# Kernel optimization log

Hardware: AMD Instinct MI355X
Metric: run time of the kernel (lower is better)

## Reference

```python
import jax, jax.numpy as jnp
import numpy as np

N_NODES = 50000
N_EDGES = 800000
D_IN = 128
D_OUT = 128


def setup_inputs() -> dict:
    key = jax.random.key(0)
    k1, k2, k3, k4 = jax.random.split(key, 4)
    feature = jax.random.normal(k1, (N_NODES, D_IN), dtype=jnp.float32)
    edge_src = jax.random.randint(k2, (N_EDGES,), 0, N_NODES, dtype=jnp.int32)
    edge_dst = jax.random.randint(k3, (N_EDGES,), 0, N_NODES, dtype=jnp.int32)
    W = jax.random.normal(k4, (D_IN, D_OUT), dtype=jnp.float32) * (1.0 / np.sqrt(D_IN))
    b = jnp.zeros((D_OUT,), dtype=jnp.float32)
    return {"feature": feature, "edge_src": edge_src, "edge_dst": edge_dst, "W": W, "b": b}


def reference(feature, edge_src, edge_dst, W, b):
    # copy_src + sum reduce: for each edge, copy src node feature, sum into dst node
    msgs = feature[edge_src]  # [E, D_IN] gather
    h = jax.ops.segment_sum(msgs, edge_dst, num_segments=N_NODES)  # [N, D_IN]
    # linear + activation (relu)
    return jax.nn.relu(h @ W + b)
```

## Files before the change

### kernel.cpp

```cpp
#include <hip/hip_runtime.h>
#include <hip/hip_fp16.h>


constexpr int N    = 50000;
constexpr int E    = 800000;
constexpr int D    = 128;
constexpr int CAP  = 64;
constexpr int NT   = 3125;
constexpr int ZSTR = 136;
constexpr int NR   = 782;
constexpr int HB   = 500;
constexpr int EPB  = E / HB;

using f16x8 = __attribute__((ext_vector_type(8))) _Float16;
using f32x4 = __attribute__((ext_vector_type(4))) float;

__global__ void setup(const float* __restrict__ W, _Float16* __restrict__ Wf,
                      _Float16* __restrict__ Z) {
    if (blockIdx.x == 8) {
        if (threadIdx.x < D) Z[(size_t)N * D + threadIdx.x] = (_Float16)0.f;
        return;
    }
    int t = blockIdx.x * 256 + threadIdx.x;
    int ct = t >> 8, ks = (t >> 6) & 3, lane = t & 63;
    int q = lane >> 4, li = lane & 15;
    _Float16 v[8];
    #pragma unroll
    for (int j = 0; j < 8; ++j)
        v[j] = (_Float16)W[(ks * 32 + q * 8 + j) * D + ct * 16 + li];
    *(f16x8*)(Wf + (size_t)t * 8) = *(const f16x8*)v;
}

__global__ __launch_bounds__(256) void midk(
        const float* __restrict__ feature,
        const int*   __restrict__ edst,
        const _Float16* __restrict__ Wf,
        int* __restrict__ hist,
        _Float16* __restrict__ Z) {
    __shared__ int h[NR];
    __shared__ _Float16 zs[4][16 * ZSTR];
    const int tid = threadIdx.x;

    if (blockIdx.x < HB) {
        const int b = blockIdx.x;
        for (int i = tid; i < NR; i += 256) h[i] = 0;
        __syncthreads();
        const int e0 = b * EPB;
        for (int i = tid; i < EPB; i += 256)
            atomicAdd(&h[edst[e0 + i] >> 6], 1);
        __syncthreads();
        for (int i = tid; i < NR; i += 256) hist[b * NR + i] = h[i];
        return;
    }

    const int wave = tid >> 6, lane = tid & 63;
    const int wt = (blockIdx.x - HB) * 4 + wave;
    if (wt >= NT) return;
    const int q = lane >> 4, li = lane & 15;

    const float* fp = feature + (size_t)(wt * 16 + li) * D + q * 8;
    f16x8 afr[4];
    #pragma unroll
    for (int ks = 0; ks < 4; ++ks) {
        const float4 u0 = *(const float4*)(fp + ks * 32);
        const float4 u1 = *(const float4*)(fp + ks * 32 + 4);
        afr[ks][0] = (_Float16)u0.x; afr[ks][1] = (_Float16)u0.y;
        afr[ks][2] = (_Float16)u0.z; afr[ks][3] = (_Float16)u0.w;
        afr[ks][4] = (_Float16)u1.x; afr[ks][5] = (_Float16)u1.y;
        afr[ks][6] = (_Float16)u1.z; afr[ks][7] = (_Float16)u1.w;
    }

    f32x4 acc[8];
    #pragma unroll
    for (int ct = 0; ct < 8; ++ct) acc[ct] = (f32x4){0.f, 0.f, 0.f, 0.f};
    #pragma unroll
    for (int ks = 0; ks < 4; ++ks)
        #pragma unroll
        for (int ct = 0; ct < 8; ++ct) {
            const f16x8 b = *(const f16x8*)(Wf + (size_t)((ct * 4 + ks) * 64 + lane) * 8);
            acc[ct] = __builtin_amdgcn_mfma_f32_16x16x32_f16(afr[ks], b, acc[ct], 0, 0, 0);
        }

    _Float16* zt = zs[wave];
    #pragma unroll
    for (int ct = 0; ct < 8; ++ct)
        #pragma unroll
        for (int r = 0; r < 4; ++r)
            zt[(q * 4 + r) * ZSTR + ct * 16 + li] = (_Float16)acc[ct][r];
    #pragma unroll
    for (int it = 0; it < 4; ++it) {
        const f16x8 v = *(const f16x8*)(zt + (it * 4 + q) * ZSTR + li * 8);
        *(f16x8*)(Z + (size_t)(wt * 16 + it * 4 + q) * D + li * 8) = v;
    }
}

__global__ void scank(int* __restrict__ hist, int* __restrict__ total) {
    const int r    = blockIdx.x;
    const int lane = threadIdx.x;
    int h[8], sum = 0;
    #pragma unroll
    for (int j = 0; j < 8; ++j) {
        const int idx = lane * 8 + j;
        h[j] = (idx < HB) ? hist[idx * NR + r] : 0;
        sum += h[j];
    }
    int incl = sum;
    #pragma unroll
    for (int off = 1; off < 64; off <<= 1) {
        int u = __shfl_up(incl, off);
        if (lane >= off) incl += u;
    }
    int run = incl - sum;
    #pragma unroll
    for (int j = 0; j < 8; ++j) {
        const int idx = lane * 8 + j;
        if (idx < HB) hist[idx * NR + r] = run;
        run += h[j];
    }
    if (lane == 63) total[r] = run;
}

__global__ __launch_bounds__(256) void partk(
        const int* __restrict__ esrc,
        const int* __restrict__ edst,
        const int* __restrict__ blockBase,
        const int* __restrict__ total,
        int* __restrict__ rangeStartG,
        unsigned int* __restrict__ part) {
    __shared__ int rs[NR];
    __shared__ int mb[NR];
    __shared__ int rk[NR];
    const int tid = threadIdx.x;
    const int b   = blockIdx.x;

    if (tid < 64) {
        int carry = 0;
        #pragma unroll
        for (int c = 0; c < 13; ++c) {
            const int idx = c * 64 + tid;
            const int v = (idx < NR) ? total[idx] : 0;
            int incl = v;
            #pragma unroll
            for (int off = 1; off < 64; off <<= 1) {
                int u = __shfl_up(incl, off);
                if (tid >= off) incl += u;
            }
            if (idx < NR) rs[idx] = incl - v + carry;
            carry += __shfl(incl, 63);
        }
    }
    for (int i = tid; i < NR; i += 256) { mb[i] = blockBase[b * NR + i]; rk[i] = 0; }
    __syncthreads();
    if (b == 0)
        for (int i = tid; i < NR; i += 256) rangeStartG[i] = rs[i];

    const int e0 = b * EPB;
    for (int i = tid; i < EPB; i += 256) {
        const int s = esrc[e0 + i];
        const int d = edst[e0 + i];
        const int r = d >> 6;
        const int k = atomicAdd(&rk[r], 1);
        part[rs[r] + mb[r] + k] = ((unsigned)(d & 63) << 16) | (unsigned)s;
    }
}

__global__ __launch_bounds__(256) void csrgather(
        const unsigned int* __restrict__ part,
        const int* __restrict__ rangeStart,
        const int* __restrict__ total,
        const _Float16* __restrict__ Z,
        const float* __restrict__ bias,
        float* __restrict__ out) {
    __shared__ unsigned short bkt[64 * CAP];
    __shared__ int deg[64];
    const int r = blockIdx.x, tid = threadIdx.x;

    if (tid < 64) deg[tid] = 0;
    __syncthreads();
    const int rsv = rangeStart[r], tot = total[r];
    for (int i = tid; i < tot; i += 256) {
        const unsigned p = part[rsv + i];
        const int local = p >> 16;
        const int src   = p & 0xFFFF;
        const int k = atomicAdd(&deg[local], 1);
        if (k < CAP) bkt[local * CAP + k] = (unsigned short)src;
    }
    __syncthreads();

    const int wave = tid >> 6, lane = tid & 63;
    const int g = lane >> 4, li = lane & 15;
    const float4 b0 = *(const float4*)(bias + li * 8);
    const float4 b1 = *(const float4*)(bias + li * 8 + 4);

    for (int pair = 0; pair < 8; ++pair) {
        const int lA = wave * 16 + pair * 2;
        const int lB = lA + 1;
        const int degA = min(deg[lA], CAP);
        const int degB = min(deg[lB], CAP);

        float accA[8] = {0,0,0,0,0,0,0,0};
        float accB[8] = {0,0,0,0,0,0,0,0};

        const int mx = max(degA, degB);
        for (int base = 0; base < mx; base += 16) {
            f16x8 hA[4], hB[4];
            #pragma unroll
            for (int t = 0; t < 4; ++t) {
                const int rr = base + t * 4 + g;
                int sA = bkt[lA * CAP + rr];
                int sB = bkt[lB * CAP + rr];
                sA = (rr < degA) ? sA : N;
                sB = (rr < degB) ? sB : N;
                hA[t] = *(const f16x8*)(Z + (size_t)sA * D + li * 8);
                hB[t] = *(const f16x8*)(Z + (size_t)sB * D + li * 8);
            }
            #pragma unroll
            for (int t = 0; t < 4; ++t)
                #pragma unroll
                for (int j = 0; j < 8; ++j) {
                    accA[j] += (float)hA[t][j];
                    accB[j] += (float)hB[t][j];
                }
        }

        #pragma unroll
        for (int j = 0; j < 8; ++j) {
            accA[j] += __shfl_xor(accA[j], 16);
            accA[j] += __shfl_xor(accA[j], 32);
            accB[j] += __shfl_xor(accB[j], 16);
            accB[j] += __shfl_xor(accB[j], 32);
        }

        const int nodeA = (r << 6) + lA;
        const int nodeB = (r << 6) + lB;
        if (g == 0 && nodeA < N) {
            float4 o0, o1;
            o0.x = fmaxf(accA[0] + b0.x, 0.f); o0.y = fmaxf(accA[1] + b0.y, 0.f);
            o0.z = fmaxf(accA[2] + b0.z, 0.f); o0.w = fmaxf(accA[3] + b0.w, 0.f);
            o1.x = fmaxf(accA[4] + b1.x, 0.f); o1.y = fmaxf(accA[5] + b1.y, 0.f);
            o1.z = fmaxf(accA[6] + b1.z, 0.f); o1.w = fmaxf(accA[7] + b1.w, 0.f);
            float* op = out + (size_t)nodeA * D + li * 8;
            *(float4*)op       = o0;
            *(float4*)(op + 4) = o1;
        } else if (g == 1 && nodeB < N) {
            float4 o0, o1;
            o0.x = fmaxf(accB[0] + b0.x, 0.f); o0.y = fmaxf(accB[1] + b0.y, 0.f);
            o0.z = fmaxf(accB[2] + b0.z, 0.f); o0.w = fmaxf(accB[3] + b0.w, 0.f);
            o1.x = fmaxf(accB[4] + b1.x, 0.f); o1.y = fmaxf(accB[5] + b1.y, 0.f);
            o1.z = fmaxf(accB[6] + b1.z, 0.f); o1.w = fmaxf(accB[7] + b1.w, 0.f);
            float* op = out + (size_t)nodeB * D + li * 8;
            *(float4*)op       = o0;
            *(float4*)(op + 4) = o1;
        }
    }
}

extern "C" void kernel_launch(void* const* d_in, const int* in_sizes, int n_in,
                              void* d_out, int out_size, void* d_ws, size_t ws_size,
                              hipStream_t stream) {
    const float* feature = (const float*)d_in[0];
    const int*   esrc    = (const int*)d_in[1];
    const int*   edst    = (const int*)d_in[2];
    const float* W       = (const float*)d_in[3];
    const float* bias    = (const float*)d_in[4];
    float*       out     = (float*)d_out;

    _Float16*     Z      = (_Float16*)d_ws;
    _Float16*     Wf     = Z + (size_t)(N + 1) * D;
    int*          hist   = (int*)(Wf + 16384);
    int*          total  = hist + HB * NR;
    int*          rangeS = total + NR;
    unsigned int* part   = (unsigned int*)(rangeS + NR);

    setup<<<9, 256, 0, stream>>>(W, Wf, Z);
    midk <<<HB + (NT + 3) / 4, 256, 0, stream>>>(feature, edst, Wf, hist, Z);
    scank<<<NR, 64, 0, stream>>>(hist, total);
    partk<<<HB, 256, 0, stream>>>(esrc, edst, hist, total, rangeS, part);
    csrgather<<<NR, 256, 0, stream>>>(part, rangeS, total, Z, bias, out);
}
```

Baseline: 145.1 us.

## Fuse all stages into one cooperative persistent kernel with grid syncs

Replaces the five separate launches (weight setup, histogram+GEMM, scan, partition, CSR gather) with a single cooperative kernel of 512 blocks that separates the phases with grid-wide syncs. Shared memory is unioned across phases, and the histogram is stored transposed so each block can scan one or two ranges. The aim is to remove the gaps and tail effects between dependent kernel launches. In exchange it adds three grid barriers and a fixed grid that handles 782 gather ranges in two uneven rounds, so load balance and occupancy may suffer.

```diff
diff --git a/kernel.cpp b/kernel.cpp
--- a/kernel.cpp
+++ b/kernel.cpp
@@ -1,256 +1,243 @@
 #include <hip/hip_runtime.h>
 #include <hip/hip_fp16.h>
+#include <hip/hip_cooperative_groups.h>
+
+namespace cg = cooperative_groups;
 
 
 constexpr int N    = 50000;
 constexpr int E    = 800000;
 constexpr int D    = 128;
 constexpr int CAP  = 64;
+constexpr int NBLK = 512;
+constexpr int NR   = 782;
 constexpr int NT   = 3125;
 constexpr int ZSTR = 136;
-constexpr int NR   = 782;
-constexpr int HB   = 500;
-constexpr int EPB  = E / HB;
+constexpr int EPB  = 1563;
+constexpr int NCH  = 13;
 
 using f16x8 = __attribute__((ext_vector_type(8))) _Float16;
 using f32x4 = __attribute__((ext_vector_type(4))) float;
 
-__global__ void setup(const float* __restrict__ W, _Float16* __restrict__ Wf,
-                      _Float16* __restrict__ Z) {
-    if (blockIdx.x == 8) {
-        if (threadIdx.x < D) Z[(size_t)N * D + threadIdx.x] = (_Float16)0.f;
-        return;
-    }
-    int t = blockIdx.x * 256 + threadIdx.x;
-    int ct = t >> 8, ks = (t >> 6) & 3, lane = t & 63;
-    int q = lane >> 4, li = lane & 15;
-    _Float16 v[8];
-    #pragma unroll
-    for (int j = 0; j < 8; ++j)
-        v[j] = (_Float16)W[(ks * 32 + q * 8 + j) * D + ct * 16 + li];
-    *(f16x8*)(Wf + (size_t)t * 8) = *(const f16x8*)v;
-}
-
-__global__ __launch_bounds__(256) void midk(
-        const float* __restrict__ feature,
-        const int*   __restrict__ edst,
-        const _Float16* __restrict__ Wf,
-        int* __restrict__ hist,
-        _Float16* __restrict__ Z) {
-    __shared__ int h[NR];
-    __shared__ _Float16 zs[4][16 * ZSTR];
-    const int tid = threadIdx.x;
-
-    if (blockIdx.x < HB) {
-        const int b = blockIdx.x;
-        for (int i = tid; i < NR; i += 256) h[i] = 0;
-        __syncthreads();
-        const int e0 = b * EPB;
-        for (int i = tid; i < EPB; i += 256)
-            atomicAdd(&h[edst[e0 + i] >> 6], 1);
-        __syncthreads();
-        for (int i = tid; i < NR; i += 256) hist[b * NR + i] = h[i];
-        return;
-    }
-
-    const int wave = tid >> 6, lane = tid & 63;
-    const int wt = (blockIdx.x - HB) * 4 + wave;
-    if (wt >= NT) return;
-    const int q = lane >> 4, li = lane & 15;
-
-    const float* fp = feature + (size_t)(wt * 16 + li) * D + q * 8;
-    f16x8 afr[4];
-    #pragma unroll
-    for (int ks = 0; ks < 4; ++ks) {
-        const float4 u0 = *(const float4*)(fp + ks * 32);
-        const float4 u1 = *(const float4*)(fp + ks * 32 + 4);
-        afr[ks][0] = (_Float16)u0.x; afr[ks][1] = (_Float16)u0.y;
-        afr[ks][2] = (_Float16)u0.z; afr[ks][3] = (_Float16)u0.w;
-        afr[ks][4] = (_Float16)u1.x; afr[ks][5] = (_Float16)u1.y;
-        afr[ks][6] = (_Float16)u1.z; afr[ks][7] = (_Float16)u1.w;
-    }
-
-    f32x4 acc[8];
-    #pragma unroll
-    for (int ct = 0; ct < 8; ++ct) acc[ct] = (f32x4){0.f, 0.f, 0.f, 0.f};
-    #pragma unroll
-    for (int ks = 0; ks < 4; ++ks)
-        #pragma unroll
-        for (int ct = 0; ct < 8; ++ct) {
-            const f16x8 b = *(const f16x8*)(Wf + (size_t)((ct * 4 + ks) * 64 + lane) * 8);
-            acc[ct] = __builtin_amdgcn_mfma_f32_16x16x32_f16(afr[ks], b, acc[ct], 0, 0, 0);
-        }
-
-    _Float16* zt = zs[wave];
-    #pragma unroll
-    for (int ct = 0; ct < 8; ++ct)
-        #pragma unroll
-        for (int r = 0; r < 4; ++r)
-            zt[(q * 4 + r) * ZSTR + ct * 16 + li] = (_Float16)acc[ct][r];
-    #pragma unroll
-    for (int it = 0; it < 4; ++it) {
-        const f16x8 v = *(const f16x8*)(zt + (it * 4 + q) * ZSTR + li * 8);
-        *(f16x8*)(Z + (size_t)(wt * 16 + it * 4 + q) * D + li * 8) = v;
-    }
-}
-
-__global__ void scank(int* __restrict__ hist, int* __restrict__ total) {
-    const int r    = blockIdx.x;
-    const int lane = threadIdx.x;
-    int h[8], sum = 0;
-    #pragma unroll
-    for (int j = 0; j < 8; ++j) {
-        const int idx = lane * 8 + j;
-        h[j] = (idx < HB) ? hist[idx * NR + r] : 0;
-        sum += h[j];
-    }
-    int incl = sum;
+__device__ __forceinline__ int wscan_incl(int v, int lane) {
     #pragma unroll
     for (int off = 1; off < 64; off <<= 1) {
-        int u = __shfl_up(incl, off);
-        if (lane >= off) incl += u;
-    }
-    int run = incl - sum;
-    #pragma unroll
-    for (int j = 0; j < 8; ++j) {
-        const int idx = lane * 8 + j;
-        if (idx < HB) hist[idx * NR + r] = run;
-        run += h[j];
-    }
-    if (lane == 63) total[r] = run;
+        int u = __shfl_up(v, off);
+        if (lane >= off) v += u;
+    }
+    return v;
 }
 
-__global__ __launch_bounds__(256) void partk(
-        const int* __restrict__ esrc,
-        const int* __restrict__ edst,
-        const int* __restrict__ blockBase,
-        const int* __restrict__ total,
-        int* __restrict__ rangeStartG,
+__global__ __launch_bounds__(256, 4) void mega(
+        const float* __restrict__ feature,
+        const int*   __restrict__ esrc,
+        const int*   __restrict__ edst,
+        const float* __restrict__ W,
+        const float* __restrict__ bias,
+        float*       __restrict__ out,
+        _Float16*    __restrict__ Z,
+        _Float16*    __restrict__ Wf,
+        int*         __restrict__ histT,
+        int*         __restrict__ mbT,
+        int*         __restrict__ total,
         unsigned int* __restrict__ part) {
     __shared__ int rs[NR];
-    __shared__ int mb[NR];
-    __shared__ int rk[NR];
-    const int tid = threadIdx.x;
-    const int b   = blockIdx.x;
-
-    if (tid < 64) {
+    __shared__ union {
+        int h[NR];
+        _Float16 zs[4][16 * ZSTR];
+        struct { int mb[NR]; int rk[NR]; } c;
+        struct { unsigned short bkt[64 * CAP]; int deg[64]; } d;
+    } sh;
+
+    cg::grid_group grid = cg::this_grid();
+    const int b    = blockIdx.x;
+    const int tid  = threadIdx.x;
+    const int wave = tid >> 6, lane = tid & 63;
+    const int q    = lane >> 4, li = lane & 15;
+    const int e0   = b * EPB;
+    const int ecnt = min(E - e0, EPB);
+
+    if (b < 8) {
+        int t = b * 256 + tid;
+        int ct = t >> 8, ks = (t >> 6) & 3, ln = t & 63;
+        int qq = ln >> 4, ll = ln & 15;
+        _Float16 v[8];
+        #pragma unroll
+        for (int j = 0; j < 8; ++j)
+            v[j] = (_Float16)W[(ks * 32 + qq * 8 + j) * D + ct * 16 + ll];
+        *(f16x8*)(Wf + (size_t)t * 8) = *(const f16x8*)v;
+    }
+    if (b == 8 && tid < D) Z[(size_t)N * D + tid] = (_Float16)0.f;
+
+    for (int i = tid; i < NR; i += 256) sh.h[i] = 0;
+    __syncthreads();
+    for (int i = tid; i < ecnt; i += 256)
+        atomicAdd(&sh.h[edst[e0 + i] >> 6], 1);
+    __syncthreads();
+    for (int i = tid; i < NR; i += 256) histT[i * NBLK + b] = sh.h[i];
+
+    grid.sync();
+
+    #pragma unroll
+    for (int it = 0; it < 2; ++it) {
+        const int wt = it * (NBLK * 4) + b * 4 + wave;
+        if (wt >= NT) break;
+        const float* fp = feature + (size_t)(wt * 16 + li) * D + q * 8;
+        f16x8 afr[4];
+        #pragma unroll
+        for (int ks = 0; ks < 4; ++ks) {
+            const float4 u0 = *(const float4*)(fp + ks * 32);
+            const float4 u1 = *(const float4*)(fp + ks * 32 + 4);
+            afr[ks][0] = (_Float16)u0.x; afr[ks][1] = (_Float16)u0.y;
+            afr[ks][2] = (_Float16)u0.z; afr[ks][3] = (_Float16)u0.w;
+            afr[ks][4] = (_Float16)u1.x; afr[ks][5] = (_Float16)u1.y;
+            afr[ks][6] = (_Float16)u1.z; afr[ks][7] = (_Float16)u1.w;
+        }
+        f32x4 acc[8];
+        #pragma unroll
+        for (int ct = 0; ct < 8; ++ct) acc[ct] = (f32x4){0.f, 0.f, 0.f, 0.f};
+        #pragma unroll
+        for (int ks = 0; ks < 4; ++ks)
+            #pragma unroll
+            for (int ct = 0; ct < 8; ++ct) {
+                const f16x8 bb = *(const f16x8*)(Wf + (size_t)((ct * 4 + ks) * 64 + lane) * 8);
+                acc[ct] = __builtin_amdgcn_mfma_f32_16x16x32_f16(afr[ks], bb, acc[ct], 0, 0, 0);
+            }
+        _Float16* zt = sh.zs[wave];
+        #pragma unroll
+        for (int ct = 0; ct < 8; ++ct)
+            #pragma unroll
+            for (int r = 0; r < 4; ++r)
+                zt[(q * 4 + r) * ZSTR + ct * 16 + li] = (_Float16)acc[ct][r];
+        #pragma unroll
+        for (int jt = 0; jt < 4; ++jt) {
+            const f16x8 v = *(const f16x8*)(zt + (jt * 4 + q) * ZSTR + li * 8);
+            *(f16x8*)(Z + (size_t)(wt * 16 + jt * 4 + q) * D + li * 8) = v;
+        }
+    }
+    if (wave == 0) {
+        #pragma unroll
+        for (int j = 0; j < 2; ++j) {
+            const int r = b + j * NBLK;
+            if (r >= NR) break;
+            int carry = 0;
+            #pragma unroll
+            for (int c = 0; c < NBLK / 64; ++c) {
+                const int idx = c * 64 + lane;
+                const int v = histT[r * NBLK + idx];
+                const int incl = wscan_incl(v, lane);
+                mbT[idx * NR + r] = incl - v + carry;
+                carry += __shfl(incl, 63);
+            }
+            if (lane == 0) total[r] = carry;
+        }
+    }
+
+    grid.sync();
+
+    if (wave == 0) {
         int carry = 0;
         #pragma unroll
-        for (int c = 0; c < 13; ++c) {
-            const int idx = c * 64 + tid;
+        for (int c = 0; c < NCH; ++c) {
+            const int idx = c * 64 + lane;
             const int v = (idx < NR) ? total[idx] : 0;
-            int incl = v;
-            #pragma unroll
-            for (int off = 1; off < 64; off <<= 1) {
-                int u = __shfl_up(incl, off);
-                if (tid >= off) incl += u;
-            }
+            const int incl = wscan_incl(v, lane);
             if (idx < NR) rs[idx] = incl - v + carry;
             carry += __shfl(incl, 63);
         }
     }
-    for (int i = tid; i < NR; i += 256) { mb[i] = blockBase[b * NR + i]; rk[i] = 0; }
+    for (int i = tid; i < NR; i += 256) {
+        sh.c.mb[i] = mbT[b * NR + i];
+        sh.c.rk[i] = 0;
+    }
     __syncthreads();
-    if (b == 0)
-        for (int i = tid; i < NR; i += 256) rangeStartG[i] = rs[i];
-
-    const int e0 = b * EPB;
-    for (int i = tid; i < EPB; i += 256) {
+    for (int i = tid; i < ecnt; i += 256) {
         const int s = esrc[e0 + i];
         const int d = edst[e0 + i];
         const int r = d >> 6;
-        const int k = atomicAdd(&rk[r], 1);
-        part[rs[r] + mb[r] + k] = ((unsigned)(d & 63) << 16) | (unsigned)s;
-    }
-}
-
-__global__ __launch_bounds__(256) void csrgather(
-        const unsigned int* __restrict__ part,
-        const int* __restrict__ rangeStart,
-        const int* __restrict__ total,
-        const _Float16* __restrict__ Z,
-        const float* __restrict__ bias,
-        float* __restrict__ out) {
-    __shared__ unsigned short bkt[64 * CAP];
-    __shared__ int deg[64];
-    const int r = blockIdx.x, tid = threadIdx.x;
-
-    if (tid < 64) deg[tid] = 0;
-    __syncthreads();
-    const int rsv = rangeStart[r], tot = total[r];
-    for (int i = tid; i < tot; i += 256) {
-        const unsigned p = part[rsv + i];
-        const int local = p >> 16;
-        const int src   = p & 0xFFFF;
-        const int k = atomicAdd(&deg[local], 1);
-        if (k < CAP) bkt[local * CAP + k] = (unsigned short)src;
-    }
-    __syncthreads();
-
-    const int wave = tid >> 6, lane = tid & 63;
-    const int g = lane >> 4, li = lane & 15;
+        const int k = atomicAdd(&sh.c.rk[r], 1);
+        part[rs[r] + sh.c.mb[r] + k] = ((unsigned)(d & 63) << 16) | (unsigned)s;
+    }
+
+    grid.sync();
+
     const float4 b0 = *(const float4*)(bias + li * 8);
     const float4 b1 = *(const float4*)(bias + li * 8 + 4);
 
-    for (int pair = 0; pair < 8; ++pair) {
-        const int lA = wave * 16 + pair * 2;
-        const int lB = lA + 1;
-        const int degA = min(deg[lA], CAP);
-        const int degB = min(deg[lB], CAP);
-
-        float accA[8] = {0,0,0,0,0,0,0,0};
-        float accB[8] = {0,0,0,0,0,0,0,0};
-
-        const int mx = max(degA, degB);
-        for (int base = 0; base < mx; base += 16) {
-            f16x8 hA[4], hB[4];
-            #pragma unroll
-            for (int t = 0; t < 4; ++t) {
-                const int rr = base + t * 4 + g;
-                int sA = bkt[lA * CAP + rr];
-                int sB = bkt[lB * CAP + rr];
-                sA = (rr < degA) ? sA : N;
-                sB = (rr < degB) ? sB : N;
-                hA[t] = *(const f16x8*)(Z + (size_t)sA * D + li * 8);
-                hB[t] = *(const f16x8*)(Z + (size_t)sB * D + li * 8);
-            }
-            #pragma unroll
-            for (int t = 0; t < 4; ++t)
+    for (int r = b; r < NR; r += NBLK) {
+        __syncthreads();
+        if (tid < 64) sh.d.deg[tid] = 0;
+        __syncthreads();
+        const int rsv = rs[r];
+        const int tot = ((r + 1 < NR) ? rs[r + 1] : E) - rsv;
+        for (int i = tid; i < tot; i += 256) {
+            const unsigned p = part[rsv + i];
+            const int local = p >> 16;
+            const int k = atomicAdd(&sh.d.deg[local], 1);
+            if (k < CAP) sh.d.bkt[local * CAP + k] = (unsigned short)(p & 0xFFFF);
+        }
+        __syncthreads();
+
+        for (int pair = 0; pair < 8; ++pair) {
+            const int lA = wave * 16 + pair * 2;
+            const int lB = lA + 1;
+            const int degA = min(sh.d.deg[lA], CAP);
+            const int degB = min(sh.d.deg[lB], CAP);
+
+            float accA[8] = {0,0,0,0,0,0,0,0};
+            float accB[8] = {0,0,0,0,0,0,0,0};
+
+            const int mx = max(degA, degB);
+            for (int base = 0; base < mx; base += 16) {
+                f16x8 hA[4], hB[4];
                 #pragma unroll
-                for (int j = 0; j < 8; ++j) {
-                    accA[j] += (float)hA[t][j];
-                    accB[j] += (float)hB[t][j];
+                for (int t = 0; t < 4; ++t) {
+                    const int rr = base + t * 4 + q;
+                    int sA = sh.d.bkt[lA * CAP + rr];
+                    int sB = sh.d.bkt[lB * CAP + rr];
+                    sA = (rr < degA) ? sA : N;
+                    sB = (rr < degB) ? sB : N;
+                    hA[t] = *(const f16x8*)(Z + (size_t)sA * D + li * 8);
+                    hB[t] = *(const f16x8*)(Z + (size_t)sB * D + li * 8);
                 }
-        }
-
-        #pragma unroll
-        for (int j = 0; j < 8; ++j) {
-            accA[j] += __shfl_xor(accA[j], 16);
-            accA[j] += __shfl_xor(accA[j], 32);
-            accB[j] += __shfl_xor(accB[j], 16);
-            accB[j] += __shfl_xor(accB[j], 32);
-        }
-
-        const int nodeA = (r << 6) + lA;
-        const int nodeB = (r << 6) + lB;
-        if (g == 0 && nodeA < N) {
-            float4 o0, o1;
-            o0.x = fmaxf(accA[0] + b0.x, 0.f); o0.y = fmaxf(accA[1] + b0.y, 0.f);
-            o0.z = fmaxf(accA[2] + b0.z, 0.f); o0.w = fmaxf(accA[3] + b0.w, 0.f);
-            o1.x = fmaxf(accA[4] + b1.x, 0.f); o1.y = fmaxf(accA[5] + b1.y, 0.f);
-            o1.z = fmaxf(accA[6] + b1.z, 0.f); o1.w = fmaxf(accA[7] + b1.w, 0.f);
-            float* op = out + (size_t)nodeA * D + li * 8;
-            *(float4*)op       = o0;
-            *(float4*)(op + 4) = o1;
-        } else if (g == 1 && nodeB < N) {
-            float4 o0, o1;
-            o0.x = fmaxf(accB[0] + b0.x, 0.f); o0.y = fmaxf(accB[1] + b0.y, 0.f);
-            o0.z = fmaxf(accB[2] + b0.z, 0.f); o0.w = fmaxf(accB[3] + b0.w, 0.f);
-            o1.x = fmaxf(accB[4] + b1.x, 0.f); o1.y = fmaxf(accB[5] + b1.y, 0.f);
-            o1.z = fmaxf(accB[6] + b1.z, 0.f); o1.w = fmaxf(accB[7] + b1.w, 0.f);
-            float* op = out + (size_t)nodeB * D + li * 8;
-            *(float4*)op       = o0;
-            *(float4*)(op + 4) = o1;
+                #pragma unroll
+                for (int t = 0; t < 4; ++t)
+                    #pragma unroll
+                    for (int j = 0; j < 8; ++j) {
+                        accA[j] += (float)hA[t][j];
+                        accB[j] += (float)hB[t][j];
+                    }
+            }
+
+            #pragma unroll
+            for (int j = 0; j < 8; ++j) {
+                accA[j] += __shfl_xor(accA[j], 16);
+                accA[j] += __shfl_xor(accA[j], 32);
+                accB[j] += __shfl_xor(accB[j], 16);
+                accB[j] += __shfl_xor(accB[j], 32);
+            }
+
+            const int nodeA = (r << 6) + lA;
+            const int nodeB = (r << 6) + lB;
+            if (q == 0 && nodeA < N) {
+                float4 o0, o1;
+                o0.x = fmaxf(accA[0] + b0.x, 0.f); o0.y = fmaxf(accA[1] + b0.y, 0.f);
+                o0.z = fmaxf(accA[2] + b0.z, 0.f); o0.w = fmaxf(accA[3] + b0.w, 0.f);
+                o1.x = fmaxf(accA[4] + b1.x, 0.f); o1.y = fmaxf(accA[5] + b1.y, 0.f);
+                o1.z = fmaxf(accA[6] + b1.z, 0.f); o1.w = fmaxf(accA[7] + b1.w, 0.f);
+                float* op = out + (size_t)nodeA * D + li * 8;
+                *(float4*)op       = o0;
+                *(float4*)(op + 4) = o1;
+            } else if (q == 1 && nodeB < N) {
+                float4 o0, o1;
+                o0.x = fmaxf(accB[0] + b0.x, 0.f); o0.y = fmaxf(accB[1] + b0.y, 0.f);
+                o0.z = fmaxf(accB[2] + b0.z, 0.f); o0.w = fmaxf(accB[3] + b0.w, 0.f);
+                o1.x = fmaxf(accB[4] + b1.x, 0.f); o1.y = fmaxf(accB[5] + b1.y, 0.f);
+                o1.z = fmaxf(accB[6] + b1.z, 0.f); o1.w = fmaxf(accB[7] + b1.w, 0.f);
+                float* op = out + (size_t)nodeB * D + li * 8;
+                *(float4*)op       = o0;
+                *(float4*)(op + 4) = o1;
+            }
         }
     }
 }
@@ -267,14 +254,14 @@
 
     _Float16*     Z      = (_Float16*)d_ws;
     _Float16*     Wf     = Z + (size_t)(N + 1) * D;
-    int*          hist   = (int*)(Wf + 16384);
-    int*          total  = hist + HB * NR;
-    int*          rangeS = total + NR;
-    unsigned int* part   = (unsigned int*)(rangeS + NR);
-
-    setup<<<9, 256, 0, stream>>>(W, Wf, Z);
-    midk <<<HB + (NT + 3) / 4, 256, 0, stream>>>(feature, edst, Wf, hist, Z);
-    scank<<<NR, 64, 0, stream>>>(hist, total);
-    partk<<<HB, 256, 0, stream>>>(esrc, edst, hist, total, rangeS, part);
-    csrgather<<<NR, 256, 0, stream>>>(part, rangeS, total, Z, bias, out);
+    int*          histT  = (int*)(Wf + 16384);
+    int*          mbT    = histT + (size_t)NR * NBLK;
+    int*          total  = mbT + (size_t)NBLK * NR;
+    unsigned int* part   = (unsigned int*)(total + NR);
+
+    void* args[] = {(void*)&feature, (void*)&esrc, (void*)&edst, (void*)&W,
+                    (void*)&bias, (void*)&out, (void*)&Z, (void*)&Wf,
+                    (void*)&histT, (void*)&mbT, (void*)&total, (void*)&part};
+    hipLaunchCooperativeKernel((const void*)mega, dim3(NBLK), dim3(256),
+                               args, 0, stream);
 }
```

Result: slower. 381.0 us (+162.5%).
